# Kernel optimization log

Measured on AMD Instinct MI355X. Metric: run time of the kernel, lower is better.

The kernel has to match this reference:

```python
import jax, jax.numpy as jnp
import numpy as np

HIDDEN = 4096
N_HEADS = 32
N_KV_HEADS = 8
HEAD_DIM = HIDDEN // N_HEADS  # 128
INTER = 11008
EPS = 1e-6
ROPE_THETA = 10000.0
B, S = 2, 2048


def setup_inputs() -> dict:
    key = jax.random.key(0)
    ks = jax.random.split(key, 8)
    sc = 0.02
    return {
        "hidden_states": jax.random.normal(ks[0], (B, S, HIDDEN), dtype=jnp.float32),
        "positions": jnp.arange(S, dtype=jnp.int32),
        "w_qkv": jax.random.normal(ks[1], (HIDDEN, (N_HEADS + 2 * N_KV_HEADS) * HEAD_DIM), dtype=jnp.float32) * sc,
        "w_o": jax.random.normal(ks[2], (N_HEADS * HEAD_DIM, HIDDEN), dtype=jnp.float32) * sc,
        "w_gate_up": jax.random.normal(ks[3], (HIDDEN, 2 * INTER), dtype=jnp.float32) * sc,
        "w_down": jax.random.normal(ks[4], (INTER, HIDDEN), dtype=jnp.float32) * sc,
        "ln1_w": jnp.ones((HIDDEN,), dtype=jnp.float32),
        "ln2_w": jnp.ones((HIDDEN,), dtype=jnp.float32),
    }


def _rms_norm(x, w):
    var = jnp.mean(jnp.square(x), axis=-1, keepdims=True)
    return x * jax.lax.rsqrt(var + EPS) * w


def _rope(x, positions):
    # x: [B, S, H, D]; NeoX-style rotary over full head_dim
    d = x.shape[-1]
    inv_freq = 1.0 / (ROPE_THETA ** (jnp.arange(0, d, 2, dtype=jnp.float32) / d))
    freqs = positions.astype(jnp.float32)[:, None] * inv_freq[None, :]  # [S, D/2]
    cos = jnp.cos(freqs)[None, :, None, :]
    sin = jnp.sin(freqs)[None, :, None, :]
    x1, x2 = jnp.split(x, 2, axis=-1)
    return jnp.concatenate([x1 * cos - x2 * sin, x2 * cos + x1 * sin], axis=-1)


def _decoder_layer(hidden_states, positions, w_qkv, w_o, w_gate_up, w_down, ln1_w, ln2_w):
    b, s, _ = hidden_states.shape
    scale = HEAD_DIM ** -0.5

    # --- attention block ---
    residual = hidden_states
    x = _rms_norm(hidden_states, ln1_w)
    qkv = x @ w_qkv
    q, k, v = jnp.split(qkv, [N_HEADS * HEAD_DIM, (N_HEADS + N_KV_HEADS) * HEAD_DIM], axis=-1)
    q = q.reshape(b, s, N_HEADS, HEAD_DIM)
    k = k.reshape(b, s, N_KV_HEADS, HEAD_DIM)
    v = v.reshape(b, s, N_KV_HEADS, HEAD_DIM)
    q = _rope(q, positions)
    k = _rope(k, positions)
    # GQA: expand kv heads
    g = N_HEADS // N_KV_HEADS
    k = jnp.repeat(k, g, axis=2)  # [B, S, H, D]
    v = jnp.repeat(v, g, axis=2)
    scores = jnp.einsum("bqhd,bkhd->bhqk", q, k) * scale
    causal = jnp.tril(jnp.ones((s, s), dtype=bool))
    scores = jnp.where(causal[None, None], scores, jnp.finfo(scores.dtype).min)
    probs = jax.nn.softmax(scores, axis=-1)
    attn = jnp.einsum("bhqk,bkhd->bqhd", probs, v).reshape(b, s, N_HEADS * HEAD_DIM)
    hidden_states = residual + attn @ w_o

    # --- MLP block (SwiGLU) ---
    residual = hidden_states
    x = _rms_norm(hidden_states, ln2_w)
    gate_up = x @ w_gate_up
    gate, up = jnp.split(gate_up, 2, axis=-1)
    hidden_states = residual + (jax.nn.silu(gate) * up) @ w_down
    return hidden_states


def reference(hidden_states, positions, w_qkv, w_o, w_gate_up, w_down, ln1_w, ln2_w):
    return _decoder_layer(hidden_states, positions, w_qkv, w_o, w_gate_up, w_down, ln1_w, ln2_w)
```

## Files before the change

kernel.cpp:

```cpp
#include <hip/hip_runtime.h>


typedef __attribute__((ext_vector_type(8))) short bf16x8;
typedef __attribute__((ext_vector_type(4))) float f32x4;

__device__ __forceinline__ ushort f2bf(float f) {
  unsigned u = __float_as_uint(f);
  return (ushort)((u + 0x7fffu + ((u >> 16) & 1u)) >> 16);
}
__device__ __forceinline__ float bf2f(ushort u) {
  union { unsigned u32; float f; } x; x.u32 = ((unsigned)u) << 16; return x.f;
}
__device__ __forceinline__ void gload16(const void* g, void* l) {
  __builtin_amdgcn_global_load_lds((__attribute__((address_space(1))) void*)g,
                                   (__attribute__((address_space(3))) void*)l,
                                   16, 0, 0);
}

#define BARRIER() asm volatile("s_barrier" ::: "memory")
#define WAIT_LGKM0() asm volatile("s_waitcnt lgkmcnt(0)" ::: "memory")
#define WAIT_VM4() asm volatile("s_waitcnt vmcnt(4)" ::: "memory")
#define WAIT_VM0() asm volatile("s_waitcnt vmcnt(0)" ::: "memory")

__global__ __launch_bounds__(256) void rmsnorm_kernel(
    const float* __restrict__ x, const float* __restrict__ g,
    ushort* __restrict__ out) {
  const int row = blockIdx.x, t = threadIdx.x;
  const float4* xp = (const float4*)(x + (size_t)row * 4096);
  float4 v[4]; float ss = 0.f;
#pragma unroll
  for (int i = 0; i < 4; ++i) {
    v[i] = xp[t + i * 256];
    ss += v[i].x * v[i].x + v[i].y * v[i].y + v[i].z * v[i].z + v[i].w * v[i].w;
  }
#pragma unroll
  for (int m = 32; m; m >>= 1) ss += __shfl_xor(ss, m);
  __shared__ float red[4];
  if ((t & 63) == 0) red[t >> 6] = ss;
  __syncthreads();
  float inv = rsqrtf((red[0] + red[1] + red[2] + red[3]) * (1.f / 4096.f) + 1e-6f);
  const float4* gp = (const float4*)g;
  ushort* op = out + (size_t)row * 4096;
#pragma unroll
  for (int i = 0; i < 4; ++i) {
    float4 gv = gp[t + i * 256];
    ushort4 o;
    o.x = f2bf(v[i].x * inv * gv.x); o.y = f2bf(v[i].y * inv * gv.y);
    o.z = f2bf(v[i].z * inv * gv.z); o.w = f2bf(v[i].w * inv * gv.w);
    *(ushort4*)(op + (size_t)(t + i * 256) * 4) = o;
  }
}

__global__ __launch_bounds__(256) void transpose_cast_kernel(
    const float* __restrict__ in, ushort* __restrict__ out,
    int ld_in, int col_off, int R) {
  __shared__ ushort tile[64][65];
  const int t = threadIdx.x;
  const int r0 = blockIdx.x * 64, c0 = blockIdx.y * 64;
  const int rl = t >> 2, cl = (t & 3) * 16;
  const float* ip = in + (size_t)(r0 + rl) * ld_in + col_off + c0 + cl;
#pragma unroll
  for (int i = 0; i < 4; ++i) {
    float4 f = ((const float4*)ip)[i];
    tile[rl][cl + i * 4 + 0] = f2bf(f.x);
    tile[rl][cl + i * 4 + 1] = f2bf(f.y);
    tile[rl][cl + i * 4 + 2] = f2bf(f.z);
    tile[rl][cl + i * 4 + 3] = f2bf(f.w);
  }
  __syncthreads();
  union { ushort us[8]; uint4 v; } pk0, pk1;
#pragma unroll
  for (int j = 0; j < 8; ++j) pk0.us[j] = tile[cl + j][rl];
#pragma unroll
  for (int j = 0; j < 8; ++j) pk1.us[j] = tile[cl + 8 + j][rl];
  uint4* op = (uint4*)(out + (size_t)(c0 + rl) * R + r0 + cl);
  op[0] = pk0.v; op[1] = pk1.v;
}

template <typename OutT, bool RES>
__global__ __launch_bounds__(512, 2) void gemm256_kernel(
    const ushort* __restrict__ A, const ushort* __restrict__ Bt,
    OutT* __restrict__ C, const float* __restrict__ res,
    int M, int N, int K) {
  extern __shared__ ushort lds[];
  ushort* Al = lds;
  ushort* Bl = lds + 32768;
  const int t = threadIdx.x, l = t & 63, w = t >> 6;
  const int wr = w >> 2, wc = w & 3;
  const int lr = l & 15, lg = l >> 4;
  const int rhi = lr >> 3, rlo = lr & 7;
  const int srow = l >> 3, sg = (l & 7) ^ srow;

  const int nby = M >> 8;
  const int nwg = (N >> 8) * nby;
  const int cpx = nwg >> 3;
  const int bid = (int)blockIdx.x;
  const int swz = (bid & 7) * cpx + (bid >> 3);
  const int m0 = (swz % nby) << 8;
  const int n0 = (swz / nby) << 8;

  const int lof0 = rhi * 512 + rlo * 64 + ((0 + lg) ^ rlo) * 8;
  const int lof1 = rhi * 512 + rlo * 64 + ((4 + lg) ^ rlo) * 8;

  const f32x4 fz = {0.f, 0.f, 0.f, 0.f};
  f32x4 acc[8][4];
#pragma unroll
  for (int i = 0; i < 8; ++i)
#pragma unroll
    for (int j = 0; j < 4; ++j) acc[i][j] = fz;
  bf16x8 a[8][2];
  bf16x8 bq[2][2];

  const ushort* Asrc = A + (size_t)(m0 + w * 8 + srow) * K + sg * 8;
  const ushort* Bsrc = Bt + (size_t)(n0 + w * 8 + srow) * K + sg * 8;
  const size_t rK64 = (size_t)64 * K, rK128 = (size_t)128 * K;
  ushort* Adst = Al + w * 512;
  ushort* Bdst = Bl + w * 512;

#define STAGE_A(buf, half, tile) do {                                   \
    const ushort* s_ = Asrc + (size_t)(half) * rK128 + ((tile) << 6);   \
    ushort* d_ = Adst + (buf) * 16384 + (half) * 8192;                  \
    gload16(s_, d_);                                                    \
    gload16(s_ + rK64, d_ + 4096);                                      \
  } while (0)
#define STAGE_B(buf, half, tile) do {                                   \
    const ushort* s_ = Bsrc + (size_t)(half) * rK128 + ((tile) << 6);   \
    ushort* d_ = Bdst + (buf) * 16384 + (half) * 8192;                  \
    gload16(s_, d_);                                                    \
    gload16(s_ + rK64, d_ + 4096);                                      \
  } while (0)
#define LDA4(AH, QM) do {                                                   \
    _Pragma("unroll") for (int mi_ = 0; mi_ < 4; ++mi_) {                   \
      a[(QM) * 4 + mi_][0] =                                                \
          *(const bf16x8*)((AH) + ((QM) * 4 + mi_) * 1024 + lof0);          \
      a[(QM) * 4 + mi_][1] =                                                \
          *(const bf16x8*)((AH) + ((QM) * 4 + mi_) * 1024 + lof1);          \
    } } while (0)
#define LDB2(BH, NQ) do {                                                   \
    _Pragma("unroll") for (int nj_ = 0; nj_ < 2; ++nj_) {                   \
      bq[nj_][0] = *(const bf16x8*)((BH) + ((NQ) * 2 + nj_) * 1024 + lof0); \
      bq[nj_][1] = *(const bf16x8*)((BH) + ((NQ) * 2 + nj_) * 1024 + lof1); \
    } } while (0)
#define MFMA16(QM, QN)                                                      \
    __builtin_amdgcn_s_setprio(1);                                          \
    _Pragma("unroll") for (int mi_ = 0; mi_ < 4; ++mi_)                     \
    _Pragma("unroll") for (int nj_ = 0; nj_ < 2; ++nj_) {                   \
      acc[(QM) * 4 + mi_][(QN) * 2 + nj_] =                                 \
          __builtin_amdgcn_mfma_f32_16x16x32_bf16(                          \
              a[(QM) * 4 + mi_][0], bq[nj_][0],                             \
              acc[(QM) * 4 + mi_][(QN) * 2 + nj_], 0, 0, 0);                \
      acc[(QM) * 4 + mi_][(QN) * 2 + nj_] =                                 \
          __builtin_amdgcn_mfma_f32_16x16x32_bf16(                          \
              a[(QM) * 4 + mi_][1], bq[nj_][1],                             \
              acc[(QM) * 4 + mi_][(QN) * 2 + nj_], 0, 0, 0);                \
    }                                                                       \
    __builtin_amdgcn_s_setprio(0);

  const ushort* A0h = Al + wr * 8192;
  const ushort* A1h = A0h + 16384;
  const ushort* B0h = Bl + (wc >> 1) * 8192 + (wc & 1) * 4096;
  const ushort* B1h = B0h + 16384;

  const int ntiles = K >> 6, nIter = K >> 7;
  STAGE_A(0, 0, 0); STAGE_A(0, 1, 0); STAGE_B(0, 0, 0); STAGE_B(0, 1, 0);
  STAGE_A(1, 0, 1); STAGE_A(1, 1, 1);
  WAIT_VM4(); BARRIER();

  for (int it = 0; it < nIter; ++it) {
    const int u = it * 2;
    LDA4(A0h, 0); LDB2(B0h, 0);
    STAGE_B(1, 0, u + 1);
    BARRIER(); WAIT_LGKM0(); MFMA16(0, 0); BARRIER();
    LDA4(A0h, 1);
    STAGE_B(1, 1, u + 1);
    BARRIER(); WAIT_LGKM0(); MFMA16(1, 0); BARRIER();
    LDB2(B0h, 1);
    if (u + 2 < ntiles) STAGE_A(0, 0, u + 2);
    BARRIER(); WAIT_LGKM0(); MFMA16(0, 1); BARRIER();
    if (u + 2 < ntiles) STAGE_A(0, 1, u + 2);
    BARRIER(); MFMA16(1, 1);
    if (u + 2 < ntiles) { WAIT_VM4(); } else { WAIT_VM0(); }
    BARRIER();
    LDA4(A1h, 0); LDB2(B1h, 0);
    if (u + 2 < ntiles) STAGE_B(0, 0, u + 2);
    BARRIER(); WAIT_LGKM0(); MFMA16(0, 0); BARRIER();
    LDA4(A1h, 1);
    if (u + 2 < ntiles) STAGE_B(0, 1, u + 2);
    BARRIER(); WAIT_LGKM0(); MFMA16(1, 0); BARRIER();
    LDB2(B1h, 1);
    if (u + 3 < ntiles) STAGE_A(1, 0, u + 3);
    BARRIER(); WAIT_LGKM0(); MFMA16(0, 1); BARRIER();
    if (u + 3 < ntiles) STAGE_A(1, 1, u + 3);
    BARRIER(); MFMA16(1, 1);
    WAIT_VM4(); BARRIER();
  }

#pragma unroll
  for (int mi = 0; mi < 8; ++mi)
#pragma unroll
    for (int ni = 0; ni < 4; ++ni)
#pragma unroll
      for (int r = 0; r < 4; ++r) {
        int row = m0 + wr * 128 + mi * 16 + lg * 4 + r;
        int col = n0 + wc * 64 + ni * 16 + lr;
        size_t idx = (size_t)row * N + col;
        float v = acc[mi][ni][r];
        if (RES) v += res[idx];
        if constexpr (sizeof(OutT) == 2) C[idx] = f2bf(v);
        else                             C[idx] = v;
      }
#undef STAGE_A
#undef STAGE_B
#undef LDA4
#undef LDB2
#undef MFMA16
}

__global__ void rope_table_kernel(const int* __restrict__ pos,
                                  float2* __restrict__ tab) {
  int idx = blockIdx.x * 256 + threadIdx.x;
  int s = idx >> 6, fi = idx & 63;
  float inv = (float)exp(-(double)(2 * fi) / 128.0 * 9.210340371976184);
  float a = (float)pos[s] * inv;
  tab[idx] = make_float2(cosf(a), sinf(a));
}

__global__ __launch_bounds__(256) void rope_scatter_kernel(
    const ushort* __restrict__ qkv, const float2* __restrict__ tab,
    ushort* __restrict__ Qr, ushort* __restrict__ Kr, ushort* __restrict__ Vt) {
  __shared__ ushort vt[64][132];
  const int t = threadIdx.x, tt = blockIdx.x, h = blockIdx.y;
  const int row = t >> 2, c = (t & 3) * 16;
  const int tok = tt * 64 + row;
  const int b = tok >> 11, s = tok & 2047;
  const ushort* ip = qkv + (size_t)tok * 6144 + h * 128;
  union U { uint4 v; ushort us[8]; };
  U a0, a1, b0, b1;
  a0.v = *(const uint4*)(ip + c);      a1.v = *(const uint4*)(ip + c + 8);
  b0.v = *(const uint4*)(ip + c + 64); b1.v = *(const uint4*)(ip + c + 72);
  if (h < 40) {
    U o0, o1, o2, o3;
#pragma unroll
    for (int j = 0; j < 8; ++j) {
      float2 cs = tab[s * 64 + c + j];
      float x1 = bf2f(a0.us[j]), x2 = bf2f(b0.us[j]);
      o0.us[j] = f2bf(x1 * cs.x - x2 * cs.y);
      o2.us[j] = f2bf(x2 * cs.x + x1 * cs.y);
    }
#pragma unroll
    for (int j = 0; j < 8; ++j) {
      float2 cs = tab[s * 64 + c + 8 + j];
      float x1 = bf2f(a1.us[j]), x2 = bf2f(b1.us[j]);
      o1.us[j] = f2bf(x1 * cs.x - x2 * cs.y);
      o3.us[j] = f2bf(x2 * cs.x + x1 * cs.y);
    }
    ushort* base;
    if (h < 32) base = Qr + ((size_t)((b * 32 + h) * 2048 + s)) * 128;
    else        base = Kr + ((size_t)((b * 8 + (h - 32)) * 2048 + s)) * 128;
    *(uint4*)(base + c)      = o0.v; *(uint4*)(base + c + 8)  = o1.v;
    *(uint4*)(base + c + 64) = o2.v; *(uint4*)(base + c + 72) = o3.v;
  } else {
    const int hv = h - 40;
#pragma unroll
    for (int j = 0; j < 8; ++j) {
      vt[row][c + j]      = a0.us[j]; vt[row][c + 8 + j]  = a1.us[j];
      vt[row][c + 64 + j] = b0.us[j]; vt[row][c + 72 + j] = b1.us[j];
    }
    __syncthreads();
    const int d = t >> 1, s0 = (t & 1) * 32, sb = (tt & 31) * 64;
    U w0, w1, w2, w3;
#pragma unroll
    for (int j = 0; j < 8; ++j) {
      w0.us[j] = vt[s0 + j][d];      w1.us[j] = vt[s0 + 8 + j][d];
      w2.us[j] = vt[s0 + 16 + j][d]; w3.us[j] = vt[s0 + 24 + j][d];
    }
    ushort* vb = Vt + ((size_t)((b * 8 + hv) * 128 + d)) * 2048 + sb + s0;
    *(uint4*)(vb) = w0.v;      *(uint4*)(vb + 8) = w1.v;
    *(uint4*)(vb + 16) = w2.v; *(uint4*)(vb + 24) = w3.v;
  }
}

__global__ __launch_bounds__(512) void attn_kernel(
    const ushort* __restrict__ Q, const ushort* __restrict__ K,
    const ushort* __restrict__ V, ushort* __restrict__ O) {
  extern __shared__ ushort sm[];
  ushort* Kl = sm;
  ushort* Vl = sm + 16384;
  ushort* Pl = sm + 32768;
  const int t = threadIdx.x, l = t & 63, w = t >> 6;
  const int lr = l & 15, lg = l >> 4;
  const int qb = blockIdx.x, h = blockIdx.y, b = blockIdx.z;
  const int hkv = h >> 2;
  const f32x4 fzero = {0.f, 0.f, 0.f, 0.f};

  const int rm = lr & 7;
  int ksw[4], vsw[2];
#pragma unroll
  for (int ks = 0; ks < 4; ++ks) ksw[ks] = ((ks * 4 + lg) ^ rm) * 8;
  vsw[0] = (lg ^ rm) * 8;
  vsw[1] = ((4 + lg) ^ rm) * 8;
  const int kcol = ((t & 15) ^ ((t >> 4) & 7)) * 8;
  const int vcol = ((t & 7) ^ ((t >> 3) & 7)) * 8;

  const float qscale = 0.08838834764831845f * 1.4426950408889634f;
  const ushort* qp =
      Q + ((size_t)((b * 32 + h) * 2048 + qb * 128 + w * 16 + lr)) * 128 + lg * 8;
  bf16x8 qf[4];
#pragma unroll
  for (int ks = 0; ks < 4; ++ks) {
    bf16x8 raw = *(const bf16x8*)(qp + ks * 32);
#pragma unroll
    for (int j = 0; j < 8; ++j)
      qf[ks][j] = (short)f2bf(bf2f((ushort)raw[j]) * qscale);
  }
  bf16x8 ones;
#pragma unroll
  for (int j = 0; j < 8; ++j) ones[j] = (short)0x3F80;
  WAIT_VM0();

  const ushort* kg = K + ((size_t)(b * 8 + hkv)) * 2048 * 128;
  const ushort* vg = V + ((size_t)(b * 8 + hkv)) * 128 * 2048;

#define STAGE_KV(buf, s0_) do {                                              \
    _Pragma("unroll") for (int i_ = 0; i_ < 2; ++i_)                         \
      gload16(kg + (size_t)((s0_) + i_ * 32 + (t >> 4)) * 128 + kcol,        \
              (char*)Kl + (buf) * 16384 + i_ * 8192 + t * 16);               \
    _Pragma("unroll") for (int i_ = 0; i_ < 2; ++i_)                         \
      gload16(vg + (size_t)(i_ * 64 + (t >> 3)) * 2048 + (s0_) + vcol,       \
              (char*)Vl + (buf) * 16384 + i_ * 8192 + t * 16);               \
  } while (0)

  f32x4 accO[8];
#pragma unroll
  for (int i = 0; i < 8; ++i) accO[i] = fzero;
  float m_r[4] = {-1e30f, -1e30f, -1e30f, -1e30f};
  float l_r[4] = {0.f, 0.f, 0.f, 0.f};
  const int qrow = qb * 128 + w * 16 + lg * 4;
  const int wrow0 = qb * 128 + w * 16;
  const int jend = 2 * qb + 1;

  STAGE_KV(0, 0);
  for (int j = 0; j <= jend; ++j) {
    if (j < jend) { STAGE_KV((j + 1) & 1, (j + 1) * 64); WAIT_VM4(); }
    else          { WAIT_VM0(); }
    BARRIER();
    const ushort* Kb = Kl + (j & 1) * 8192;
    const ushort* Vb = Vl + (j & 1) * 8192;

    f32x4 sc[4];
#pragma unroll
    for (int ni = 0; ni < 4; ++ni) sc[ni] = fzero;
    __builtin_amdgcn_s_setprio(1);
#pragma unroll
    for (int ni = 0; ni < 4; ++ni)
#pragma unroll
      for (int ks = 0; ks < 4; ++ks) {
        bf16x8 kf = *(const bf16x8*)(Kb + (ni * 16 + lr) * 128 + ksw[ks]);
        sc[ni] = __builtin_amdgcn_mfma_f32_16x16x32_bf16(qf[ks], kf, sc[ni], 0, 0, 0);
      }
    __builtin_amdgcn_s_setprio(0);
    if (j * 64 + 63 > wrow0) {
#pragma unroll
      for (int ni = 0; ni < 4; ++ni)
#pragma unroll
        for (int r = 0; r < 4; ++r)
          if (j * 64 + ni * 16 + lr > qrow + r) sc[ni][r] = -1e30f;
    }
    float mx[4];
#pragma unroll
    for (int r = 0; r < 4; ++r) {
      float v = fmaxf(fmaxf(sc[0][r], sc[1][r]), fmaxf(sc[2][r], sc[3][r]));
#pragma unroll
      for (int m = 8; m; m >>= 1) v = fmaxf(v, __shfl_xor(v, m));
      mx[r] = v;
    }
    bool ok = mx[0] <= m_r[0] + 8.f && mx[1] <= m_r[1] + 8.f &&
              mx[2] <= m_r[2] + 8.f && mx[3] <= m_r[3] + 8.f;
    if (!__all(ok)) {
#pragma unroll
      for (int r = 0; r < 4; ++r) {
        float mnew = fmaxf(m_r[r], mx[r]);
        float fsc = exp2f(m_r[r] - mnew);
        l_r[r] *= fsc;
        m_r[r] = mnew;
#pragma unroll
        for (int i = 0; i < 8; ++i) accO[i][r] *= fsc;
      }
    }
#pragma unroll
    for (int ni = 0; ni < 4; ++ni)
#pragma unroll
      for (int r = 0; r < 4; ++r) {
        int prow = w * 16 + lg * 4 + r;
        int slot = (ni * 2 + (lr >> 3)) ^ (prow & 7);
        Pl[prow * 64 + slot * 8 + rm] = f2bf(exp2f(sc[ni][r] - m_r[r]));
      }
    WAIT_LGKM0();
    f32x4 accL = fzero;
    __builtin_amdgcn_s_setprio(1);
#pragma unroll
    for (int ks = 0; ks < 2; ++ks) {
      bf16x8 pf = *(const bf16x8*)(Pl + (w * 16 + lr) * 64 + vsw[ks]);
#pragma unroll
      for (int nf = 0; nf < 8; ++nf) {
        bf16x8 vf = *(const bf16x8*)(Vb + (nf * 16 + lr) * 64 + vsw[ks]);
        accO[nf] = __builtin_amdgcn_mfma_f32_16x16x32_bf16(pf, vf, accO[nf], 0, 0, 0);
      }
      accL = __builtin_amdgcn_mfma_f32_16x16x32_bf16(pf, ones, accL, 0, 0, 0);
    }
    __builtin_amdgcn_s_setprio(0);
#pragma unroll
    for (int r = 0; r < 4; ++r) l_r[r] += accL[r];
    BARRIER();
  }
#undef STAGE_KV
  float invl[4];
#pragma unroll
  for (int r = 0; r < 4; ++r) invl[r] = 1.f / l_r[r];
#pragma unroll
  for (int nf = 0; nf < 8; ++nf)
#pragma unroll
    for (int r = 0; r < 4; ++r) {
      int q = qb * 128 + w * 16 + lg * 4 + r;
      int d = nf * 16 + lr;
      O[((size_t)(b * 2048 + q)) * 4096 + h * 128 + d] = f2bf(accO[nf][r] * invl[r]);
    }
}

__global__ void swiglu_kernel(ushort* __restrict__ gate,
                              const ushort* __restrict__ up, int n8) {
  union U { uint4 v; ushort us[8]; };
  for (int i = blockIdx.x * blockDim.x + threadIdx.x; i < n8;
       i += gridDim.x * blockDim.x) {
    U gv, uv, ov;
    gv.v = ((const uint4*)gate)[i];
    uv.v = ((const uint4*)up)[i];
#pragma unroll
    for (int j = 0; j < 8; ++j) {
      float x = bf2f(gv.us[j]);
      float y = bf2f(uv.us[j]);
      ov.us[j] = f2bf(x / (1.f + __expf(-x)) * y);
    }
    ((uint4*)gate)[i] = ov.v;
  }
}

#define OFF_W    ((size_t)0)
#define OFF_H1   ((size_t)90177536)
#define OFF_XN   ((size_t)157286400)
#define OFF_QKV  ((size_t)190840832)
#define OFF_TAB  ((size_t)241172480)
#define OFF_QR   ((size_t)242221056)
#define OFF_KR   ((size_t)275775488)
#define OFF_VT   ((size_t)284164096)
#define OFF_ATTN ((size_t)292552704)
#define OFF_GATE OFF_QKV
#define OFF_UP   ((size_t)326107136)
#define WS_NEED  ((size_t)416284672)

extern "C" void kernel_launch(void* const* d_in, const int* in_sizes, int n_in,
                              void* d_out, int out_size, void* d_ws,
                              size_t ws_size, hipStream_t stream) {
  (void)in_sizes; (void)n_in; (void)out_size;
  if (ws_size < WS_NEED) return;
  const float* hs     = (const float*)d_in[0];
  const int*   pos    = (const int*)d_in[1];
  const float* w_qkv  = (const float*)d_in[2];
  const float* w_o    = (const float*)d_in[3];
  const float* w_gu   = (const float*)d_in[4];
  const float* w_down = (const float*)d_in[5];
  const float* ln1    = (const float*)d_in[6];
  const float* ln2    = (const float*)d_in[7];
  float* out = (float*)d_out;
  char* ws = (char*)d_ws;

  ushort* W    = (ushort*)(ws + OFF_W);
  float*  h1   = (float*)(ws + OFF_H1);
  ushort* xn   = (ushort*)(ws + OFF_XN);
  ushort* qkv  = (ushort*)(ws + OFF_QKV);
  float2* tab  = (float2*)(ws + OFF_TAB);
  ushort* Qr   = (ushort*)(ws + OFF_QR);
  ushort* Kr   = (ushort*)(ws + OFF_KR);
  ushort* Vt   = (ushort*)(ws + OFF_VT);
  ushort* attn = (ushort*)(ws + OFF_ATTN);
  ushort* gate = (ushort*)(ws + OFF_GATE);
  ushort* up   = (ushort*)(ws + OFF_UP);

  auto kb = gemm256_kernel<ushort, false>;
  auto kf = gemm256_kernel<float, true>;
  hipFuncSetAttribute((const void*)kb, hipFuncAttributeMaxDynamicSharedMemorySize, 131072);
  hipFuncSetAttribute((const void*)kf, hipFuncAttributeMaxDynamicSharedMemorySize, 131072);
  hipFuncSetAttribute((const void*)attn_kernel, hipFuncAttributeMaxDynamicSharedMemorySize, 81920);

  rmsnorm_kernel<<<4096, 256, 0, stream>>>(hs, ln1, xn);
  transpose_cast_kernel<<<dim3(64, 96), 256, 0, stream>>>(w_qkv, W, 6144, 0, 4096);
  gemm256_kernel<ushort, false><<<384, 512, 131072, stream>>>(
      xn, W, qkv, nullptr, 4096, 6144, 4096);
  rope_table_kernel<<<512, 256, 0, stream>>>(pos, tab);
  rope_scatter_kernel<<<dim3(64, 48), 256, 0, stream>>>(qkv, tab, Qr, Kr, Vt);
  attn_kernel<<<dim3(16, 32, 2), 512, 81920, stream>>>(Qr, Kr, Vt, attn);
  transpose_cast_kernel<<<dim3(64, 64), 256, 0, stream>>>(w_o, W, 4096, 0, 4096);
  gemm256_kernel<float, true><<<256, 512, 131072, stream>>>(
      attn, W, h1, hs, 4096, 4096, 4096);

  rmsnorm_kernel<<<4096, 256, 0, stream>>>(h1, ln2, xn);
  transpose_cast_kernel<<<dim3(64, 172), 256, 0, stream>>>(w_gu, W, 22016, 0, 4096);
  gemm256_kernel<ushort, false><<<688, 512, 131072, stream>>>(
      xn, W, gate, nullptr, 4096, 11008, 4096);
  transpose_cast_kernel<<<dim3(64, 172), 256, 0, stream>>>(w_gu, W, 22016, 11008, 4096);
  gemm256_kernel<ushort, false><<<688, 512, 131072, stream>>>(
      xn, W, up, nullptr, 4096, 11008, 4096);
  swiglu_kernel<<<2048, 256, 0, stream>>>(gate, up, (4096 * 11008) / 8);
  transpose_cast_kernel<<<dim3(172, 64), 256, 0, stream>>>(w_down, W, 4096, 0, 11008);
  gemm256_kernel<float, true><<<256, 512, 131072, stream>>>(
      gate, W, out, h1, 4096, 4096, 11008);
}
```

Before: 1.811 ms.

## Fuse gate and up GEMMs with SwiGLU epilogue into one kernel

```diff
diff --git a/kernel.cpp b/kernel.cpp
--- a/kernel.cpp
+++ b/kernel.cpp
@@ -19,6 +19,7 @@
 
 #define BARRIER() asm volatile("s_barrier" ::: "memory")
 #define WAIT_LGKM0() asm volatile("s_waitcnt lgkmcnt(0)" ::: "memory")
+#define WAIT_VM6() asm volatile("s_waitcnt vmcnt(6)" ::: "memory")
 #define WAIT_VM4() asm volatile("s_waitcnt vmcnt(4)" ::: "memory")
 #define WAIT_VM0() asm volatile("s_waitcnt vmcnt(0)" ::: "memory")
 
@@ -216,6 +217,134 @@
 #undef MFMA16
 }
 
+__global__ __launch_bounds__(512, 2) void gemm256_gateup_kernel(
+    const ushort* __restrict__ A, const ushort* __restrict__ Bg,
+    const ushort* __restrict__ Bu, ushort* __restrict__ C,
+    int M, int N, int K) {
+  extern __shared__ ushort lds[];
+  ushort* Al  = lds;
+  ushort* Bgl = lds + 16384;
+  ushort* Bul = lds + 49152;
+  const int t = threadIdx.x, l = t & 63, w = t >> 6;
+  const int wr = w >> 2, wc = w & 3;
+  const int lr = l & 15, lg = l >> 4;
+  const int rhi = lr >> 3, rlo = lr & 7;
+  const int srow = l >> 3, sg = (l & 7) ^ srow;
+
+  const int nby = M >> 7;
+  const int nwg = (N >> 8) * nby;
+  const int cpx = nwg >> 3;
+  const int bid = (int)blockIdx.x;
+  const int swz = (bid & 7) * cpx + (bid >> 3);
+  const int m0 = (swz % nby) << 7;
+  const int n0 = (swz / nby) << 8;
+
+  const int lof0 = rhi * 512 + rlo * 64 + ((0 + lg) ^ rlo) * 8;
+  const int lof1 = rhi * 512 + rlo * 64 + ((4 + lg) ^ rlo) * 8;
+
+  const f32x4 fz = {0.f, 0.f, 0.f, 0.f};
+  f32x4 accg[4][4], accu[4][4];
+#pragma unroll
+  for (int i = 0; i < 4; ++i)
+#pragma unroll
+    for (int j = 0; j < 4; ++j) { accg[i][j] = fz; accu[i][j] = fz; }
+  bf16x8 a[4][2];
+  bf16x8 bq[2][2];
+
+  const ushort* Asrc  = A  + (size_t)(m0 + w * 8 + srow) * K + sg * 8;
+  const ushort* Bgsrc = Bg + (size_t)(n0 + w * 8 + srow) * K + sg * 8;
+  const ushort* Busrc = Bu + (size_t)(n0 + w * 8 + srow) * K + sg * 8;
+  const size_t rK64 = (size_t)64 * K;
+  ushort* Adst  = Al  + w * 512;
+  ushort* Bgdst = Bgl + w * 512;
+  ushort* Budst = Bul + w * 512;
+
+#define GU_STAGE_A2(buf, tile) do {                                     \
+    const ushort* s_ = Asrc + ((tile) << 6);                            \
+    ushort* d_ = Adst + (buf) * 8192;                                   \
+    gload16(s_, d_); gload16(s_ + rK64, d_ + 4096);                     \
+  } while (0)
+#define GU_STAGE_BG4(buf, tile) do {                                    \
+    const ushort* s_ = Bgsrc + ((tile) << 6);                           \
+    ushort* d_ = Bgdst + (buf) * 16384;                                 \
+    gload16(s_, d_);             gload16(s_ + rK64, d_ + 4096);         \
+    gload16(s_ + 2 * rK64, d_ + 8192); gload16(s_ + 3 * rK64, d_ + 12288); \
+  } while (0)
+#define GU_STAGE_BU4(tile) do {                                         \
+    const ushort* s_ = Busrc + ((tile) << 6);                           \
+    gload16(s_, Budst);              gload16(s_ + rK64, Budst + 4096);  \
+    gload16(s_ + 2 * rK64, Budst + 8192);                               \
+    gload16(s_ + 3 * rK64, Budst + 12288);                              \
+  } while (0)
+#define GU_LDA8(AH) do {                                                    \
+    _Pragma("unroll") for (int mi_ = 0; mi_ < 4; ++mi_) {                   \
+      a[mi_][0] = *(const bf16x8*)((AH) + mi_ * 1024 + lof0);               \
+      a[mi_][1] = *(const bf16x8*)((AH) + mi_ * 1024 + lof1);               \
+    } } while (0)
+#define GU_LDB2(BH, NQ) do {                                                \
+    _Pragma("unroll") for (int nj_ = 0; nj_ < 2; ++nj_) {                   \
+      bq[nj_][0] = *(const bf16x8*)((BH) + ((NQ) * 2 + nj_) * 1024 + lof0); \
+      bq[nj_][1] = *(const bf16x8*)((BH) + ((NQ) * 2 + nj_) * 1024 + lof1); \
+    } } while (0)
+#define GU_MFMA16(ACC, QN)                                                  \
+    __builtin_amdgcn_s_setprio(1);                                          \
+    _Pragma("unroll") for (int mi_ = 0; mi_ < 4; ++mi_)                     \
+    _Pragma("unroll") for (int nj_ = 0; nj_ < 2; ++nj_) {                   \
+      ACC[mi_][(QN) * 2 + nj_] =                                            \
+          __builtin_amdgcn_mfma_f32_16x16x32_bf16(                          \
+              a[mi_][0], bq[nj_][0], ACC[mi_][(QN) * 2 + nj_], 0, 0, 0);    \
+      ACC[mi_][(QN) * 2 + nj_] =                                            \
+          __builtin_amdgcn_mfma_f32_16x16x32_bf16(                          \
+              a[mi_][1], bq[nj_][1], ACC[mi_][(QN) * 2 + nj_], 0, 0, 0);    \
+    }                                                                       \
+    __builtin_amdgcn_s_setprio(0);
+
+  const int nt = K >> 6;
+  GU_STAGE_A2(0, 0); GU_STAGE_BG4(0, 0); GU_STAGE_BU4(0);
+  WAIT_VM0(); BARRIER();
+
+  for (int u = 0; u < nt; ++u) {
+    const int buf = u & 1;
+    const ushort* Ah  = Al  + buf * 8192  + wr * 4096;
+    const ushort* Bgh = Bgl + buf * 16384 + wc * 4096;
+    const ushort* Buh = Bul + wc * 4096;
+    const bool more = (u + 1 < nt);
+    if (more) { GU_STAGE_A2(buf ^ 1, u + 1); GU_STAGE_BG4(buf ^ 1, u + 1); }
+    GU_LDA8(Ah); GU_LDB2(Bgh, 0);
+    BARRIER(); WAIT_LGKM0(); GU_MFMA16(accg, 0); BARRIER();
+    GU_LDB2(Bgh, 1);
+    BARRIER(); WAIT_LGKM0(); GU_MFMA16(accg, 1); BARRIER();
+    if (more) { WAIT_VM6(); } else { WAIT_VM0(); }
+    BARRIER();
+    GU_LDB2(Buh, 0);
+    BARRIER(); WAIT_LGKM0(); GU_MFMA16(accu, 0); BARRIER();
+    GU_LDB2(Buh, 1);
+    BARRIER(); WAIT_LGKM0(); GU_MFMA16(accu, 1); BARRIER();
+    if (more) { GU_STAGE_BU4(u + 1); WAIT_VM4(); }
+    BARRIER();
+  }
+
+#pragma unroll
+  for (int mi = 0; mi < 4; ++mi)
+#pragma unroll
+    for (int ni = 0; ni < 4; ++ni)
+#pragma unroll
+      for (int r = 0; r < 4; ++r) {
+        int row = m0 + wr * 64 + mi * 16 + lg * 4 + r;
+        int col = n0 + wc * 64 + ni * 16 + lr;
+        size_t idx = (size_t)row * N + col;
+        float g = accg[mi][ni][r];
+        float s = g / (1.f + __expf(-g));
+        C[idx] = f2bf(s * accu[mi][ni][r]);
+      }
+#undef GU_STAGE_A2
+#undef GU_STAGE_BG4
+#undef GU_STAGE_BU4
+#undef GU_LDA8
+#undef GU_LDB2
+#undef GU_MFMA16
+}
+
 __global__ void rope_table_kernel(const int* __restrict__ pos,
                                   float2* __restrict__ tab) {
   int idx = blockIdx.x * 256 + threadIdx.x;
@@ -427,24 +556,6 @@
     }
 }
 
-__global__ void swiglu_kernel(ushort* __restrict__ gate,
-                              const ushort* __restrict__ up, int n8) {
-  union U { uint4 v; ushort us[8]; };
-  for (int i = blockIdx.x * blockDim.x + threadIdx.x; i < n8;
-       i += gridDim.x * blockDim.x) {
-    U gv, uv, ov;
-    gv.v = ((const uint4*)gate)[i];
-    uv.v = ((const uint4*)up)[i];
-#pragma unroll
-    for (int j = 0; j < 8; ++j) {
-      float x = bf2f(gv.us[j]);
-      float y = bf2f(uv.us[j]);
-      ov.us[j] = f2bf(x / (1.f + __expf(-x)) * y);
-    }
-    ((uint4*)gate)[i] = ov.v;
-  }
-}
-
 #define OFF_W    ((size_t)0)
 #define OFF_H1   ((size_t)90177536)
 #define OFF_XN   ((size_t)157286400)
@@ -454,7 +565,7 @@
 #define OFF_KR   ((size_t)275775488)
 #define OFF_VT   ((size_t)284164096)
 #define OFF_ATTN ((size_t)292552704)
-#define OFF_GATE OFF_QKV
+#define OFF_W2   OFF_QKV
 #define OFF_UP   ((size_t)326107136)
 #define WS_NEED  ((size_t)416284672)
 
@@ -475,6 +586,7 @@
   char* ws = (char*)d_ws;
 
   ushort* W    = (ushort*)(ws + OFF_W);
+  ushort* W2   = (ushort*)(ws + OFF_W2);
   float*  h1   = (float*)(ws + OFF_H1);
   ushort* xn   = (ushort*)(ws + OFF_XN);
   ushort* qkv  = (ushort*)(ws + OFF_QKV);
@@ -483,13 +595,13 @@
   ushort* Kr   = (ushort*)(ws + OFF_KR);
   ushort* Vt   = (ushort*)(ws + OFF_VT);
   ushort* attn = (ushort*)(ws + OFF_ATTN);
-  ushort* gate = (ushort*)(ws + OFF_GATE);
-  ushort* up   = (ushort*)(ws + OFF_UP);
+  ushort* act  = (ushort*)(ws + OFF_UP);
 
   auto kb = gemm256_kernel<ushort, false>;
   auto kf = gemm256_kernel<float, true>;
   hipFuncSetAttribute((const void*)kb, hipFuncAttributeMaxDynamicSharedMemorySize, 131072);
   hipFuncSetAttribute((const void*)kf, hipFuncAttributeMaxDynamicSharedMemorySize, 131072);
+  hipFuncSetAttribute((const void*)gemm256_gateup_kernel, hipFuncAttributeMaxDynamicSharedMemorySize, 131072);
   hipFuncSetAttribute((const void*)attn_kernel, hipFuncAttributeMaxDynamicSharedMemorySize, 81920);
 
   rmsnorm_kernel<<<4096, 256, 0, stream>>>(hs, ln1, xn);
@@ -505,13 +617,10 @@
 
   rmsnorm_kernel<<<4096, 256, 0, stream>>>(h1, ln2, xn);
   transpose_cast_kernel<<<dim3(64, 172), 256, 0, stream>>>(w_gu, W, 22016, 0, 4096);
-  gemm256_kernel<ushort, false><<<688, 512, 131072, stream>>>(
-      xn, W, gate, nullptr, 4096, 11008, 4096);
-  transpose_cast_kernel<<<dim3(64, 172), 256, 0, stream>>>(w_gu, W, 22016, 11008, 4096);
-  gemm256_kernel<ushort, false><<<688, 512, 131072, stream>>>(
-      xn, W, up, nullptr, 4096, 11008, 4096);
-  swiglu_kernel<<<2048, 256, 0, stream>>>(gate, up, (4096 * 11008) / 8);
+  transpose_cast_kernel<<<dim3(64, 172), 256, 0, stream>>>(w_gu, W2, 22016, 11008, 4096);
+  gemm256_gateup_kernel<<<1376, 512, 131072, stream>>>(
+      xn, W, W2, act, 4096, 11008, 4096);
   transpose_cast_kernel<<<dim3(172, 64), 256, 0, stream>>>(w_down, W, 4096, 0, 11008);
   gemm256_kernel<float, true><<<256, 512, 131072, stream>>>(
-      gate, W, out, h1, 4096, 4096, 11008);
-}
+      act, W, out, h1, 4096, 4096, 11008);
+}
```

After: 1.965 ms. 1.09x slower.
